# Kernel tuning notes

Hardware: AMD Instinct MI355X
Metric: run time of the kernel (lower is better)

Reference implementation:

```python
import jax, jax.numpy as jnp
import numpy as np

RADIUS = 0.12   # init_kwargs radius
NSAMPLE = 32    # init_kwargs nsample
USE_XYZ = True  # init_kwargs use_xyz


def ball_query(xyz, new_xyz, radius, nsample):
    """xyz: (B,N,3), new_xyz: (B,M,3) -> idx (B,M,nsample) int32.
    PointNet++ semantics: first `nsample` points (in index order) within
    `radius` of each query; slots past the count are padded with the first
    found index."""
    B, N, _ = xyz.shape
    # squared distances (B, M, N) -- the dominant intermediate
    d2 = jnp.sum((new_xyz[:, :, None, :] - xyz[:, None, :, :]) ** 2, axis=-1)
    mask = d2 < radius * radius
    # score so that earlier in-ball indices have higher score; out-of-ball = 0
    score = jnp.where(mask, (N - jnp.arange(N, dtype=jnp.int32)), 0)
    _, idx = jax.lax.top_k(score, nsample)            # (B, M, nsample)
    valid = jnp.take_along_axis(mask, idx, axis=-1)   # which slots are real hits
    idx = jnp.where(valid, idx, idx[..., :1])         # pad with first found index
    return idx


def group_points(feat, idx):
    """feat: (B,C,N), idx: (B,M,S) -> (B,C,M,S) gather along N."""
    B, C, N = feat.shape
    M, S = idx.shape[1], idx.shape[2]
    idx_flat = jnp.broadcast_to(idx.reshape(B, 1, M * S), (B, C, M * S))
    out = jnp.take_along_axis(feat, idx_flat, axis=2)
    return out.reshape(B, C, M, S)


def setup_inputs() -> dict:
    key = jax.random.key(0)
    k1, k2 = jax.random.split(key)
    B, N, M, C = 4, 8192, 4096, 64
    xyz = jax.random.uniform(k1, (B, N, 3), dtype=jnp.float32)  # points in unit cube
    new_xyz = xyz[:, :M, :]                                      # FPS-like subset of points
    features = jax.random.normal(k2, (B, C, N), dtype=jnp.float32)
    return {"xyz": xyz, "new_xyz": new_xyz, "features": features}


def reference(xyz, new_xyz, features):
    idx = ball_query(xyz, new_xyz, RADIUS, NSAMPLE)             # (B,M,S)
    xyz_t = jnp.transpose(xyz, (0, 2, 1))                        # (B,3,N)
    grouped_xyz = group_points(xyz_t, idx)                       # (B,3,M,S)
    grouped_xyz = grouped_xyz - jnp.transpose(new_xyz, (0, 2, 1))[..., None]
    grouped_feat = group_points(features, idx)                   # (B,C,M,S)
    if USE_XYZ:
        new_features = jnp.concatenate([grouped_xyz, grouped_feat], axis=1)
    else:
        new_features = grouped_feat
    return new_features  # (B, 3+C, M, S)
```

## Files before the change

kernel.cpp:

```cpp
#include <hip/hip_runtime.h>
#include <cstdint>
#include <cstddef>

#define BB 4
#define NN 8192
#define MM 4096
#define CC 64
#define SS 32
#define CH 67
#define NC 512
#define RMARG 0.1201f

__device__ __constant__ float kRR = (float)(0.12 * 0.12);

__device__ __forceinline__ int cell_of(float x, float y, float z) {
    const int ix = min((int)(x * 8.0f), 7);
    const int iy = min((int)(y * 8.0f), 7);
    const int iz = min((int)(z * 8.0f), 7);
    return (ix << 6) + (iy << 3) + iz;
}

__global__ __launch_bounds__(256) void k_zero(int* __restrict__ cnts) {
    const int i = blockIdx.x * blockDim.x + threadIdx.x;
    if (i < BB * NC) cnts[i] = 0;
}

__global__ __launch_bounds__(256) void k_count(const float* __restrict__ xyz,
                                               int* __restrict__ cnts) {
    const int p = blockIdx.x * blockDim.x + threadIdx.x;
    if (p >= BB * NN) return;
    const int b = p >> 13;
    const float x = xyz[(size_t)p * 3 + 0];
    const float y = xyz[(size_t)p * 3 + 1];
    const float z = xyz[(size_t)p * 3 + 2];
    atomicAdd(&cnts[b * NC + cell_of(x, y, z)], 1);
}

__global__ __launch_bounds__(512) void k_scan(const int* __restrict__ cnts,
                                              int* __restrict__ cellStart,
                                              int* __restrict__ ptr) {
    __shared__ int sm[NC];
    const int t = (int)threadIdx.x;
    const int b = (int)blockIdx.x;
    const int v = cnts[b * NC + t];
    sm[t] = v;
    __syncthreads();
    for (int d = 1; d < NC; d <<= 1) {
        const int u = (t >= d) ? sm[t - d] : 0;
        __syncthreads();
        sm[t] += u;
        __syncthreads();
    }
    cellStart[b * (NC + 1) + t + 1] = sm[t];
    if (t == 0) cellStart[b * (NC + 1)] = 0;
    ptr[b * NC + t] = sm[t] - v;
}

__global__ __launch_bounds__(256) void k_scatter(const float* __restrict__ xyz,
                                                 int* __restrict__ ptr,
                                                 float4* __restrict__ pk) {
    const int p = blockIdx.x * blockDim.x + threadIdx.x;
    if (p >= BB * NN) return;
    const int b = p >> 13;
    const int n = p & (NN - 1);
    const float x = xyz[(size_t)p * 3 + 0];
    const float y = xyz[(size_t)p * 3 + 1];
    const float z = xyz[(size_t)p * 3 + 2];
    const int pos = atomicAdd(&ptr[b * NC + cell_of(x, y, z)], 1);
    pk[b * NN + pos] = make_float4(x, y, z, __int_as_float(n));
}

__global__ __launch_bounds__(256) void transpose_feat(const float* __restrict__ feat,
                                                      float* __restrict__ ft) {
    __shared__ float tile[64][65];
    const int blk = blockIdx.x;
    const int b = blk / (NN / 64);
    const int n0 = (blk % (NN / 64)) * 64;
    const int tn = (int)(threadIdx.x & 63);
    const int q = (int)(threadIdx.x >> 6);
    const float* fb = feat + (size_t)b * CC * NN;
    #pragma unroll
    for (int k = 0; k < 16; ++k) {
        const int c = q * 16 + k;
        tile[tn][c] = fb[(size_t)c * NN + n0 + tn];
    }
    __syncthreads();
    float* fo = ft + ((size_t)b * NN + n0) * CC;
    #pragma unroll
    for (int k = 0; k < 16; ++k) {
        const int rn = q * 16 + k;
        fo[(size_t)rn * CC + tn] = tile[rn][tn];
    }
}

__global__ __launch_bounds__(256) void qg_grid_kernel(
    const float4* __restrict__ pk,
    const int* __restrict__ cellStart,
    const float* __restrict__ ft,
    const float* __restrict__ xyz,
    const float* __restrict__ new_xyz,
    float* __restrict__ out)
{
    __shared__ unsigned int bm[4][NN / 32];
    __shared__ int slots_sm[4][SS];

    const int tid = (int)threadIdx.x;
    const int lane = tid & 63;
    const int w = tid >> 6;
    const int wave = (int)blockIdx.x * 4 + w;
    const int b = wave >> 12;
    const int m = wave & (MM - 1);

    unsigned int* __restrict__ bitmap = bm[w];
    int* __restrict__ slot = slots_sm[w];

    #pragma unroll
    for (int k = 0; k < 4; ++k) bitmap[(k << 6) + lane] = 0u;

    const float* __restrict__ xb = xyz + (size_t)b * NN * 3;
    const size_t qoff = ((size_t)b * MM + m) * 3;
    const float cx = new_xyz[qoff + 0];
    const float cy = new_xyz[qoff + 1];
    const float cz = new_xyz[qoff + 2];
    const float rr = kRR;

    const int x0 = max(0, (int)((cx - RMARG) * 8.0f));
    const int x1 = min(7, (int)((cx + RMARG) * 8.0f));
    const int y0 = max(0, (int)((cy - RMARG) * 8.0f));
    const int y1 = min(7, (int)((cy + RMARG) * 8.0f));
    const int z0 = max(0, (int)((cz - RMARG) * 8.0f));
    const int z1 = min(7, (int)((cz + RMARG) * 8.0f));

    const int* __restrict__ cs = cellStart + b * (NC + 1);
    const float4* __restrict__ pb = pk + b * NN;

    for (int ix = x0; ix <= x1; ++ix) {
        for (int iy = y0; iy <= y1; ++iy) {
            const int cbase = (ix << 6) + (iy << 3);
            const int beg = cs[cbase + z0];
            const int end = cs[cbase + z1 + 1];
            for (int off = beg; off < end; off += 64) {
                const int a = off + lane;
                const bool act = a < end;
                const float4 v = pb[act ? a : beg];
                const float dx = __fsub_rn(v.x, cx);
                const float dy = __fsub_rn(v.y, cy);
                const float dz = __fsub_rn(v.z, cz);
                const float d2 = __fadd_rn(__fadd_rn(__fmul_rn(dx, dx), __fmul_rn(dy, dy)),
                                           __fmul_rn(dz, dz));
                if (act && d2 < rr) {
                    const int n = __float_as_int(v.w);
                    atomicOr(&bitmap[n >> 5], 1u << (n & 31));
                }
            }
        }
    }

    const uint4 wv = *reinterpret_cast<const uint4*>(&bitmap[lane << 2]);
    const int pc = __popc(wv.x) + __popc(wv.y) + __popc(wv.z) + __popc(wv.w);
    int incl = pc;
    #pragma unroll
    for (int d = 1; d < 64; d <<= 1) {
        const int t = __shfl_up(incl, d);
        if (lane >= d) incl += t;
    }
    const int K = __shfl(incl, 63);
    int r = incl - pc;
    if (r < SS) {
        const int base = lane << 7;
        unsigned int mw0 = wv.x, mw1 = wv.y, mw2 = wv.z, mw3 = wv.w;
        while (mw0 && r < SS) { slot[r++] = base +  0 + __builtin_ctz(mw0); mw0 &= mw0 - 1; }
        while (mw1 && r < SS) { slot[r++] = base + 32 + __builtin_ctz(mw1); mw1 &= mw1 - 1; }
        while (mw2 && r < SS) { slot[r++] = base + 64 + __builtin_ctz(mw2); mw2 &= mw2 - 1; }
        while (mw3 && r < SS) { slot[r++] = base + 96 + __builtin_ctz(mw3); mw3 &= mw3 - 1; }
    }

    const int s = lane & 31;
    const int h = lane >> 5;
    const int Kc = (K < SS) ? K : SS;
    int n_of;
    if (Kc == 0) n_of = 0;
    else n_of = (s < Kc) ? slot[s] : slot[0];

    const size_t obase = ((size_t)b * CH) * (size_t)(MM * SS) + (size_t)m * SS + s;

    if (h == 0) {
        const float* xr = xb + (size_t)n_of * 3;
        out[obase + 0 * (size_t)(MM * SS)] = __fsub_rn(xr[0], cx);
        out[obase + 1 * (size_t)(MM * SS)] = __fsub_rn(xr[1], cy);
        out[obase + 2 * (size_t)(MM * SS)] = __fsub_rn(xr[2], cz);
    }
    const float4* fr4 = (const float4*)(ft + ((size_t)b * NN + n_of) * CC + (h << 5));
    float4 f[8];
    #pragma unroll
    for (int j = 0; j < 8; ++j) f[j] = fr4[j];
    #pragma unroll
    for (int j = 0; j < 8; ++j) {
        const size_t cb = obase + (size_t)(3 + (h << 5) + (j << 2)) * (size_t)(MM * SS);
        out[cb + 0 * (size_t)(MM * SS)] = f[j].x;
        out[cb + 1 * (size_t)(MM * SS)] = f[j].y;
        out[cb + 2 * (size_t)(MM * SS)] = f[j].z;
        out[cb + 3 * (size_t)(MM * SS)] = f[j].w;
    }
}

__global__ __launch_bounds__(256) void qg_fused_kernel(
    const float* __restrict__ xyz, const float* __restrict__ new_xyz,
    const float* __restrict__ feat, float* __restrict__ out)
{
    const int wave = (int)((blockIdx.x * blockDim.x + threadIdx.x) >> 6);
    const int lane = (int)(threadIdx.x & 63);
    const int b = wave / MM;
    const int m = wave % MM;

    const float* __restrict__ xb = xyz + (size_t)b * NN * 3;
    const size_t qoff = ((size_t)b * MM + m) * 3;
    const float cx = new_xyz[qoff + 0];
    const float cy = new_xyz[qoff + 1];
    const float cz = new_xyz[qoff + 2];
    const float rr = kRR;

    int my_nb = -1;
    int cnt = 0;

    for (int base = 0; base < NN; base += 512) {
        float px[8], py[8], pz[8];
        #pragma unroll
        for (int k = 0; k < 8; ++k) {
            const int i = base + (k << 6) + lane;
            px[k] = xb[i * 3 + 0]; py[k] = xb[i * 3 + 1]; pz[k] = xb[i * 3 + 2];
        }
        #pragma unroll
        for (int k = 0; k < 8; ++k) {
            const float dx = __fsub_rn(px[k], cx);
            const float dy = __fsub_rn(py[k], cy);
            const float dz = __fsub_rn(pz[k], cz);
            const float d2 = __fadd_rn(__fadd_rn(__fmul_rn(dx, dx), __fmul_rn(dy, dy)),
                                       __fmul_rn(dz, dz));
            const bool hit = d2 < rr;
            const unsigned long long mask = __ballot(hit);
            const int pc = __popcll(mask);
            if (pc) {
                const int rank = cnt + (int)__popcll(mask & ((1ull << lane) - 1ull));
                const int addr = (hit && rank < 63) ? rank : 63;
                const int recv = __builtin_amdgcn_ds_permute(addr << 2,
                                                             base + (k << 6) + lane);
                if (lane >= cnt && lane < SS && (lane - cnt) < pc) my_nb = recv;
                cnt += pc;
                if (cnt >= SS) break;
            }
        }
        if (cnt >= SS) break;
    }

    int first = __shfl(my_nb, 0);
    if (first < 0) first = 0;
    if (lane < SS && my_nb < 0) my_nb = first;
    const int n_of = __shfl(my_nb, lane & 31);

    const int s = lane & 31;
    const int h = lane >> 5;
    const size_t obase = ((size_t)b * CH) * (size_t)(MM * SS) + (size_t)m * SS + s;
    const float* __restrict__ fb = feat + (size_t)b * CC * NN;
    #pragma unroll 2
    for (int cc = 0; cc < CH + 1; cc += 2) {
        const int c = cc + h;
        if (c < CH) {
            float v;
            if (c < 3) {
                const float center = (c == 0) ? cx : (c == 1) ? cy : cz;
                v = __fsub_rn(xb[(size_t)n_of * 3 + c], center);
            } else {
                v = fb[(size_t)(c - 3) * NN + n_of];
            }
            out[obase + (size_t)c * (size_t)(MM * SS)] = v;
        }
    }
}

extern "C" void kernel_launch(void* const* d_in, const int* in_sizes, int n_in,
                              void* d_out, int out_size, void* d_ws, size_t ws_size,
                              hipStream_t stream) {
    const float* xyz     = (const float*)d_in[0];
    const float* new_xyz = (const float*)d_in[1];
    const float* feat    = (const float*)d_in[2];
    float* out = (float*)d_out;

    const size_t ft_b = (size_t)BB * NN * CC * sizeof(float);
    float*  ft     = (float*)d_ws;
    int*    cnts   = (int*)((char*)d_ws + ft_b);
    int*    cellSt = cnts + BB * NC;
    int*    ptr    = cellSt + BB * (NC + 1);
    int*    pad    = ptr + BB * NC;
    float4* pk     = (float4*)(((uintptr_t)pad + 15) & ~(uintptr_t)15);
    const size_t need = ((char*)(pk + BB * NN) - (char*)d_ws);

    if (ws_size >= need) {
        k_zero<<<(BB * NC + 255) / 256, 256, 0, stream>>>(cnts);
        k_count<<<(BB * NN + 255) / 256, 256, 0, stream>>>(xyz, cnts);
        k_scan<<<BB, NC, 0, stream>>>(cnts, cellSt, ptr);
        k_scatter<<<(BB * NN + 255) / 256, 256, 0, stream>>>(xyz, ptr, pk);
        transpose_feat<<<BB * (NN / 64), 256, 0, stream>>>(feat, ft);
        qg_grid_kernel<<<(BB * MM) / 4, 256, 0, stream>>>(pk, cellSt, ft, xyz,
                                                          new_xyz, out);
    } else {
        qg_fused_kernel<<<(BB * MM) / 4, 256, 0, stream>>>(xyz, new_xyz, feat, out);
    }
}
```

Measured before the change: 71.35 us.

## Fuse grid build and feature transpose into one prep kernel

Replaces five preprocessing launches (zero, count, scan, scatter, transpose) with a single 1024-thread kernel. The first BB blocks each build one batch's cell grid entirely in shared memory: counting with shared atomics, scanning, and scattering from register-held points. The remaining blocks perform the feature transpose. This removes four launch gaps and the global atomics and round trips, at the cost of serializing each batch's grid build inside one block, which may become the long pole.

```diff
diff --git a/kernel.cpp b/kernel.cpp
--- a/kernel.cpp
+++ b/kernel.cpp
@@ -20,76 +20,82 @@
     return (ix << 6) + (iy << 3) + iz;
 }
 
-__global__ __launch_bounds__(256) void k_zero(int* __restrict__ cnts) {
-    const int i = blockIdx.x * blockDim.x + threadIdx.x;
-    if (i < BB * NC) cnts[i] = 0;
-}
-
-__global__ __launch_bounds__(256) void k_count(const float* __restrict__ xyz,
-                                               int* __restrict__ cnts) {
-    const int p = blockIdx.x * blockDim.x + threadIdx.x;
-    if (p >= BB * NN) return;
-    const int b = p >> 13;
-    const float x = xyz[(size_t)p * 3 + 0];
-    const float y = xyz[(size_t)p * 3 + 1];
-    const float z = xyz[(size_t)p * 3 + 2];
-    atomicAdd(&cnts[b * NC + cell_of(x, y, z)], 1);
-}
-
-__global__ __launch_bounds__(512) void k_scan(const int* __restrict__ cnts,
-                                              int* __restrict__ cellStart,
-                                              int* __restrict__ ptr) {
-    __shared__ int sm[NC];
-    const int t = (int)threadIdx.x;
-    const int b = (int)blockIdx.x;
-    const int v = cnts[b * NC + t];
-    sm[t] = v;
-    __syncthreads();
-    for (int d = 1; d < NC; d <<= 1) {
-        const int u = (t >= d) ? sm[t - d] : 0;
+__global__ __launch_bounds__(1024) void k_prep(
+    const float* __restrict__ xyz,
+    const float* __restrict__ feat,
+    float* __restrict__ ft,
+    int* __restrict__ cellStart,
+    float4* __restrict__ pk)
+{
+    __shared__ __align__(16) char smem[64 * 65 * sizeof(float)];
+    const int blk = (int)blockIdx.x;
+    const int tid = (int)threadIdx.x;
+
+    if (blk < BB) {
+        int* sm  = (int*)smem;
+        int* cur = sm + NC;
+        const int b = blk;
+
+        if (tid < NC) sm[tid] = 0;
         __syncthreads();
-        sm[t] += u;
+
+        float xs[8], ys[8], zs[8];
+        int cl[8];
+        const float* __restrict__ xb = xyz + (size_t)b * NN * 3;
+        #pragma unroll
+        for (int k = 0; k < 8; ++k) {
+            const int n = (k << 10) + tid;
+            xs[k] = xb[n * 3 + 0];
+            ys[k] = xb[n * 3 + 1];
+            zs[k] = xb[n * 3 + 2];
+            cl[k] = cell_of(xs[k], ys[k], zs[k]);
+            atomicAdd(&sm[cl[k]], 1);
+        }
         __syncthreads();
-    }
-    cellStart[b * (NC + 1) + t + 1] = sm[t];
-    if (t == 0) cellStart[b * (NC + 1)] = 0;
-    ptr[b * NC + t] = sm[t] - v;
-}
-
-__global__ __launch_bounds__(256) void k_scatter(const float* __restrict__ xyz,
-                                                 int* __restrict__ ptr,
-                                                 float4* __restrict__ pk) {
-    const int p = blockIdx.x * blockDim.x + threadIdx.x;
-    if (p >= BB * NN) return;
-    const int b = p >> 13;
-    const int n = p & (NN - 1);
-    const float x = xyz[(size_t)p * 3 + 0];
-    const float y = xyz[(size_t)p * 3 + 1];
-    const float z = xyz[(size_t)p * 3 + 2];
-    const int pos = atomicAdd(&ptr[b * NC + cell_of(x, y, z)], 1);
-    pk[b * NN + pos] = make_float4(x, y, z, __int_as_float(n));
-}
-
-__global__ __launch_bounds__(256) void transpose_feat(const float* __restrict__ feat,
-                                                      float* __restrict__ ft) {
-    __shared__ float tile[64][65];
-    const int blk = blockIdx.x;
-    const int b = blk / (NN / 64);
-    const int n0 = (blk % (NN / 64)) * 64;
-    const int tn = (int)(threadIdx.x & 63);
-    const int q = (int)(threadIdx.x >> 6);
-    const float* fb = feat + (size_t)b * CC * NN;
-    #pragma unroll
-    for (int k = 0; k < 16; ++k) {
-        const int c = q * 16 + k;
-        tile[tn][c] = fb[(size_t)c * NN + n0 + tn];
-    }
-    __syncthreads();
-    float* fo = ft + ((size_t)b * NN + n0) * CC;
-    #pragma unroll
-    for (int k = 0; k < 16; ++k) {
-        const int rn = q * 16 + k;
-        fo[(size_t)rn * CC + tn] = tile[rn][tn];
+
+        int v = 0;
+        if (tid < NC) v = sm[tid];
+        for (int d = 1; d < NC; d <<= 1) {
+            int u = 0;
+            if (tid < NC && tid >= d) u = sm[tid - d];
+            __syncthreads();
+            if (tid < NC) sm[tid] += u;
+            __syncthreads();
+        }
+        if (tid < NC) {
+            const int inc = sm[tid];
+            cellStart[b * (NC + 1) + tid + 1] = inc;
+            cur[tid] = inc - v;
+            if (tid == 0) cellStart[b * (NC + 1)] = 0;
+        }
+        __syncthreads();
+
+        #pragma unroll
+        for (int k = 0; k < 8; ++k) {
+            const int n = (k << 10) + tid;
+            const int pos = atomicAdd(&cur[cl[k]], 1);
+            pk[b * NN + pos] = make_float4(xs[k], ys[k], zs[k], __int_as_float(n));
+        }
+    } else {
+        float (*tile)[65] = (float(*)[65])smem;
+        const int blk2 = blk - BB;
+        const int b = blk2 / (NN / 64);
+        const int n0 = (blk2 % (NN / 64)) * 64;
+        const int tn = tid & 63;
+        const int q = tid >> 6;
+        const float* __restrict__ fb = feat + (size_t)b * CC * NN;
+        #pragma unroll
+        for (int k = 0; k < 4; ++k) {
+            const int c = (q << 2) + k;
+            tile[tn][c] = fb[(size_t)c * NN + n0 + tn];
+        }
+        __syncthreads();
+        float* fo = ft + ((size_t)b * NN + n0) * CC;
+        #pragma unroll
+        for (int k = 0; k < 4; ++k) {
+            const int rn = (q << 2) + k;
+            fo[(size_t)rn * CC + tn] = tile[rn][tn];
+        }
     }
 }
 
@@ -288,19 +294,13 @@
 
     const size_t ft_b = (size_t)BB * NN * CC * sizeof(float);
     float*  ft     = (float*)d_ws;
-    int*    cnts   = (int*)((char*)d_ws + ft_b);
-    int*    cellSt = cnts + BB * NC;
-    int*    ptr    = cellSt + BB * (NC + 1);
-    int*    pad    = ptr + BB * NC;
-    float4* pk     = (float4*)(((uintptr_t)pad + 15) & ~(uintptr_t)15);
+    int*    cellSt = (int*)((char*)d_ws + ft_b);
+    char*   after  = (char*)(cellSt + BB * (NC + 1));
+    float4* pk     = (float4*)(((uintptr_t)after + 15) & ~(uintptr_t)15);
     const size_t need = ((char*)(pk + BB * NN) - (char*)d_ws);
 
     if (ws_size >= need) {
-        k_zero<<<(BB * NC + 255) / 256, 256, 0, stream>>>(cnts);
-        k_count<<<(BB * NN + 255) / 256, 256, 0, stream>>>(xyz, cnts);
-        k_scan<<<BB, NC, 0, stream>>>(cnts, cellSt, ptr);
-        k_scatter<<<(BB * NN + 255) / 256, 256, 0, stream>>>(xyz, ptr, pk);
-        transpose_feat<<<BB * (NN / 64), 256, 0, stream>>>(feat, ft);
+        k_prep<<<BB + BB * (NN / 64), 1024, 0, stream>>>(xyz, feat, ft, cellSt, pk);
         qg_grid_kernel<<<(BB * MM) / 4, 256, 0, stream>>>(pk, cellSt, ft, xyz,
                                                           new_xyz, out);
     } else {
```

Result: faster. 60.86 us (-14.7%).
